# Kernel tuning notes

Measured on AMD Instinct MI355X. Metric: run time of the kernel, lower is better.

## Reference

```python
import jax, jax.numpy as jnp
import numpy as np

N_HEAD, N_KV, HEAD_DIM, GATE_CH = 16, 4, 128, 32

def _rope(x, cos, sin):
    d = x.shape[3] // 2
    x1, x2 = x[..., :d], x[..., d:]
    return jnp.concatenate([x1 * cos + x2 * sin, x1 * (-sin) + x2 * cos], axis=3)

def _rmsnorm(x):
    xf = x.astype(jnp.float32)
    return (x * jax.lax.rsqrt(jnp.mean(xf * xf, axis=-1, keepdims=True) + 1e-6)).astype(x.dtype)

def setup_inputs() -> dict:
    key = jax.random.key(0)
    ks = jax.random.split(key, 9)
    B, T, C = 2, 2048, 2048
    return {
        "x":  jax.random.normal(ks[0], (B, T, C), jnp.float32),
        "ve": jax.random.normal(ks[1], (B, T, N_KV * HEAD_DIM), jnp.float32),
        "cos": jax.random.uniform(ks[2], (T, 1, HEAD_DIM // 2), jnp.float32),
        "sin": jax.random.uniform(ks[3], (T, 1, HEAD_DIM // 2), jnp.float32),
        "Wq": jax.random.normal(ks[4], (C, N_HEAD * HEAD_DIM), jnp.float32) * 0.02,
        "Wk": jax.random.normal(ks[5], (C, N_KV * HEAD_DIM), jnp.float32) * 0.02,
        "Wv": jax.random.normal(ks[6], (C, N_KV * HEAD_DIM), jnp.float32) * 0.02,
        "Wg": jax.random.normal(ks[7], (GATE_CH, N_KV), jnp.float32) * 0.02,
        "Wo": jax.random.normal(ks[8], (C, C), jnp.float32) * 0.02,
        "window": 1024,
    }

def reference(x, ve, cos, sin, Wq, Wk, Wv, Wg, Wo, window):
    B, T, C = x.shape
    q = (x @ Wq).reshape(B, T, N_HEAD, HEAD_DIM)
    k = (x @ Wk).reshape(B, T, N_KV, HEAD_DIM)
    v = (x @ Wv).reshape(B, T, N_KV, HEAD_DIM)
    # value-embedding gate (ve_gate active for this layer)
    gate = 2.0 * jax.nn.sigmoid(x[..., :GATE_CH] @ Wg)  # (B,T,N_KV)
    v = v + gate[..., None] * ve.reshape(B, T, N_KV, HEAD_DIM)
    q, k = _rope(q, cos, sin), _rope(k, cos, sin)
    q, k = _rmsnorm(q), _rmsnorm(k)
    # GQA: repeat kv heads (repeat_interleave over head dim)
    groups = N_HEAD // N_KV
    k = jnp.repeat(k, groups, axis=2)
    v = jnp.repeat(v, groups, axis=2)
    scale = 1.0 / np.sqrt(HEAD_DIM)
    scores = jnp.einsum("bthd,bshd->bhts", q, k) * scale  # (B,H,T,T)
    idx = jnp.arange(T)
    diff = idx[None, :] - idx[:, None]  # diff[i,j] = j - i, as in torch code
    mask = (diff >= 0) & (diff < window)
    scores = jnp.where(mask[None, None], scores, -jnp.inf)
    p = jax.nn.softmax(scores, axis=-1)
    y = jnp.einsum("bhts,bshd->bthd", p, v).reshape(B, T, C)
    return y @ Wo
```

## Files before the change

kernel.cpp:

```cpp
#include <hip/hip_runtime.h>
#include <hip/hip_bf16.h>
#include <cstdint>

typedef __hip_bfloat16 bf16;
typedef __attribute__((ext_vector_type(8))) short short8;
typedef __attribute__((ext_vector_type(4))) float f32x4;

#define T_   2048
#define CDIM 2048
#define NH   16
#define NKV  4
#define HD   128
#define QSCALE (0.08838834764831845f * 1.44269504088896340f)

__device__ __forceinline__ void gload_lds16(const void* g, void* l) {
  __builtin_amdgcn_global_load_lds(
      (const __attribute__((address_space(1))) void*)g,
      (__attribute__((address_space(3))) void*)l, 16, 0, 0);
}

__global__ __launch_bounds__(256) void cast_x_kernel(const float4* __restrict__ in,
                                                     ushort4* __restrict__ out, int n4) {
  int i = blockIdx.x * 256 + threadIdx.x;
  if (i >= n4) return;
  float4 v = in[i];
  union { bf16 h[4]; ushort4 u; } cv;
  cv.h[0] = __float2bfloat16(v.x);
  cv.h[1] = __float2bfloat16(v.y);
  cv.h[2] = __float2bfloat16(v.z);
  cv.h[3] = __float2bfloat16(v.w);
  out[i] = cv.u;
}

__global__ __launch_bounds__(256) void cast_transpose(const float* __restrict__ W,
                                                      bf16* __restrict__ WT,
                                                      int K, int N) {
  __shared__ float tile[32][33];
  int k0 = blockIdx.y * 32, n0 = blockIdx.x * 32;
  int r = threadIdx.x >> 5, c = threadIdx.x & 31;
  for (int i = 0; i < 4; ++i)
    tile[r + i * 8][c] = W[(size_t)(k0 + r + i * 8) * N + n0 + c];
  __syncthreads();
  for (int i = 0; i < 4; ++i)
    WT[(size_t)(n0 + r + i * 8) * K + k0 + c] = __float2bfloat16(tile[c][r + i * 8]);
}

template <int MREP, typename CT>
__global__ __launch_bounds__(512, 2) void gemm_8p(const bf16* __restrict__ A,
                                                  const bf16* __restrict__ BT,
                                                  CT* __restrict__ C,
                                                  int N, int K, int RY, int RX) {
  constexpr int BM = MREP * 32;
  constexpr int ALOADS = BM / 64;
  __shared__ __align__(16) bf16 sA[2][BM * 64];
  __shared__ __align__(16) bf16 sB[2][256 * 64];

  int tid = threadIdx.x;
  int lane = tid & 63, w = tid >> 6;
  int wm = w >> 2, wn = w & 3;
  int lr = lane & 15, lk = lane >> 4;

  int xcd = blockIdx.x & 7, t = blockIdx.x >> 3;
  int by = (xcd >> 1) * RY + t / RX;
  int bx = (xcd & 1) * RX + t % RX;
  int m0 = by * BM, n0 = bx * 256;

  f32x4 acc[MREP][4];
#pragma unroll
  for (int m = 0; m < MREP; ++m)
#pragma unroll
    for (int n = 0; n < 4; ++n) acc[m][n] = (f32x4){0.f, 0.f, 0.f, 0.f};

  const bf16* Abase = A + (size_t)m0 * K;
  const bf16* Bbase = BT + (size_t)n0 * K;

  auto stage = [&](int b, int kt) {
    int kb = kt << 6;
#pragma unroll
    for (int i = 0; i < ALOADS; ++i) {
      int c = i * 512 + tid;
      int r = c >> 3, sl = c & 7;
      gload_lds16(Abase + (size_t)r * K + kb + ((sl ^ (r & 7)) << 3),
                  (char*)(&sA[b][0]) + c * 16);
    }
#pragma unroll
    for (int i = 0; i < 4; ++i) {
      int c = i * 512 + tid;
      int r = c >> 3, sl = c & 7;
      gload_lds16(Bbase + (size_t)r * K + kb + ((sl ^ (r & 7)) << 3),
                  (char*)(&sB[b][0]) + c * 16);
    }
  };

  int nk = K >> 6;
  stage(0, 0);
  stage(1, 1);
  if constexpr (MREP == 8)
    asm volatile("s_waitcnt vmcnt(8)\n\ts_barrier" ::: "memory");
  else
    asm volatile("s_waitcnt vmcnt(6)\n\ts_barrier" ::: "memory");

  for (int kt = 0; kt < nk; ++kt) {
    int d = kt & 1;
    const char* sAb = (const char*)(&sA[d][0]);
    const char* sBb = (const char*)(&sB[d][0]);

    short8 bfr[4][2];
#pragma unroll
    for (int n = 0; n < 4; ++n) {
      int row = wn * 64 + n * 16 + lr;
      const char* rb = sBb + row * 128;
      int rx = (row & 7) << 4;
      bfr[n][0] = *(const short8*)(rb + ((lk * 16) ^ rx));
      bfr[n][1] = *(const short8*)(rb + ((64 + lk * 16) ^ rx));
    }

#pragma unroll
    for (int p = 0; p < MREP / 2; ++p) {
      short8 af[2][2];
#pragma unroll
      for (int mi = 0; mi < 2; ++mi) {
        int row = wm * (MREP * 16) + (p * 2 + mi) * 16 + lr;
        const char* rb = sAb + row * 128;
        int rx = (row & 7) << 4;
        af[mi][0] = *(const short8*)(rb + ((lk * 16) ^ rx));
        af[mi][1] = *(const short8*)(rb + ((64 + lk * 16) ^ rx));
      }
      __builtin_amdgcn_s_setprio(1);
#pragma unroll
      for (int kk = 0; kk < 2; ++kk)
#pragma unroll
        for (int mi = 0; mi < 2; ++mi)
#pragma unroll
          for (int n = 0; n < 4; ++n)
            acc[p * 2 + mi][n] = __builtin_amdgcn_mfma_f32_16x16x32_bf16(
                af[mi][kk], bfr[n][kk], acc[p * 2 + mi][n], 0, 0, 0);
      __builtin_amdgcn_s_setprio(0);
    }

    asm volatile("s_waitcnt lgkmcnt(0)\n\ts_barrier" ::: "memory");
    if (kt + 2 < nk) {
      stage(d, kt + 2);
      if constexpr (MREP == 8)
        asm volatile("s_waitcnt vmcnt(8)\n\ts_barrier" ::: "memory");
      else
        asm volatile("s_waitcnt vmcnt(6)\n\ts_barrier" ::: "memory");
    } else {
      asm volatile("s_waitcnt vmcnt(0)\n\ts_barrier" ::: "memory");
    }
  }

#pragma unroll
  for (int m = 0; m < MREP; ++m)
#pragma unroll
    for (int n = 0; n < 4; ++n)
#pragma unroll
      for (int jj = 0; jj < 4; ++jj) {
        size_t idx = (size_t)(m0 + wm * (MREP * 16) + m * 16 + lk * 4 + jj) * N +
                     n0 + wn * 64 + n * 16 + lr;
        if constexpr (__is_same(CT, float))
          C[idx] = acc[m][n][jj];
        else
          C[idx] = __float2bfloat16(acc[m][n][jj]);
      }
}

__global__ __launch_bounds__(256) void epilogue_kernel(
    const bf16* __restrict__ qkv, const float* __restrict__ x,
    const float* __restrict__ ve, const float* __restrict__ cosT,
    const float* __restrict__ sinT, const float* __restrict__ Wg,
    bf16* __restrict__ qn, bf16* __restrict__ kn, bf16* __restrict__ vT) {
  int row = blockIdx.x;
  int bi = row >> 11, t = row & 2047;
  int tid = threadIdx.x, lane = tid & 63, w = tid >> 6;
  __shared__ float gate[NKV];
  size_t rb = (size_t)row * 3072;

  if (tid < 128) {
    int g = tid >> 5, i = tid & 31;
    float p = x[(size_t)row * CDIM + i] * Wg[i * 4 + g];
    p += __shfl_xor(p, 1);  p += __shfl_xor(p, 2);
    p += __shfl_xor(p, 4);  p += __shfl_xor(p, 8);
    p += __shfl_xor(p, 16);
    if (i == 0) gate[g] = 2.f / (1.f + __expf(-p));
  }
  __syncthreads();

  float cv = cosT[t * 64 + lane];
  float sv = sinT[t * 64 + lane];

  for (int it = 0; it < 4; ++it) {
    int h = it * 4 + w;
    float x1 = __bfloat162float(qkv[rb + h * 128 + lane]);
    float x2 = __bfloat162float(qkv[rb + h * 128 + 64 + lane]);
    float y1 = x1 * cv + x2 * sv;
    float y2 = x2 * cv - x1 * sv;
    float ss = y1 * y1 + y2 * y2;
    ss += __shfl_xor(ss, 1);  ss += __shfl_xor(ss, 2);  ss += __shfl_xor(ss, 4);
    ss += __shfl_xor(ss, 8);  ss += __shfl_xor(ss, 16); ss += __shfl_xor(ss, 32);
    float r = rsqrtf(ss * (1.f / 128.f) + 1e-6f) * QSCALE;
    size_t ob = (size_t)row * (NH * HD) + h * 128;
    qn[ob + lane] = __float2bfloat16(y1 * r);
    qn[ob + 64 + lane] = __float2bfloat16(y2 * r);
  }
  {
    int h = w;
    float x1 = __bfloat162float(qkv[rb + 2048 + h * 128 + lane]);
    float x2 = __bfloat162float(qkv[rb + 2048 + h * 128 + 64 + lane]);
    float y1 = x1 * cv + x2 * sv;
    float y2 = x2 * cv - x1 * sv;
    float ss = y1 * y1 + y2 * y2;
    ss += __shfl_xor(ss, 1);  ss += __shfl_xor(ss, 2);  ss += __shfl_xor(ss, 4);
    ss += __shfl_xor(ss, 8);  ss += __shfl_xor(ss, 16); ss += __shfl_xor(ss, 32);
    float r = rsqrtf(ss * (1.f / 128.f) + 1e-6f);
    size_t ob = (size_t)row * (NKV * HD) + h * 128;
    kn[ob + lane] = __float2bfloat16(y1 * r);
    kn[ob + 64 + lane] = __float2bfloat16(y2 * r);
  }
  for (int e = tid; e < 512; e += 256) {
    int kv = e >> 7, d = e & 127;
    float val = __bfloat162float(qkv[rb + 2560 + e]) + gate[kv] * ve[(size_t)row * 512 + e];
    vT[((size_t)(bi * NKV + kv) * HD + d) * T_ + t] = __float2bfloat16(val);
  }
}

__global__ __launch_bounds__(256) void attn_kernel(
    const bf16* __restrict__ qn, const bf16* __restrict__ kn,
    const bf16* __restrict__ vT, bf16* __restrict__ y,
    const int* __restrict__ winp) {
  __shared__ __align__(16) bf16 sK[2][64 * 128];
  __shared__ __align__(16) bf16 sV[2][128 * 64];
  __shared__ __align__(16) bf16 sP[4][16 * 64];

  int win = *winp;
  int id = blockIdx.x;
  int g  = id & 7;
  int bi = g >> 2;
  int kvh = g & 3;
  int rem = id >> 3;
  int h  = kvh * 4 + (rem & 3);
  int jslot = (rem >> 2) & 7;
  int s5 = rem >> 5;
  int q0i = (s5 == 0) ? (2 * jslot) : (s5 == 1) ? (2 * jslot + 1)
          : (s5 == 2) ? (16 + jslot) : (31 - jslot);
  int q0 = q0i << 6;
  int tid = threadIdx.x;
  int lane = tid & 63, w = tid >> 6;
  int lr = lane & 15, lk = lane >> 4;

  short8 qf[4];
  {
    const bf16* qrow = qn + (size_t)(bi * T_ + q0 + w * 16 + lr) * (NH * HD) + h * HD;
    for (int c = 0; c < 4; ++c) qf[c] = *(const short8*)(qrow + c * 32 + lk * 8);
  }

  f32x4 o[8];
  for (int i = 0; i < 8; ++i) o[i] = (f32x4){0.f, 0.f, 0.f, 0.f};
  float lpart[4] = {0.f, 0.f, 0.f, 0.f};

  int jt0 = q0 >> 6;
  int hi = q0 + 62 + win; if (hi > T_ - 1) hi = T_ - 1;
  int jt1 = hi >> 6;
  const float NEGINF = -__builtin_inff();

  char* sPb = (char*)(&sP[w][0]);
  int prx = (lr & 7) << 4;

  auto stageKV = [&](int b, int jtx) {
    int j0x = jtx << 6;
    for (int i = 0; i < 4; ++i) {
      int c = i * 256 + tid;
      int r = c >> 4, sl = c & 15;
      gload_lds16(kn + (size_t)(bi * T_ + j0x + r) * (NKV * HD) + kvh * HD + ((sl ^ (r & 7)) * 8),
                  (char*)(&sK[b][0]) + c * 16);
    }
    for (int i = 0; i < 4; ++i) {
      int c = i * 256 + tid;
      int r = c >> 3, sl = c & 7;
      gload_lds16(vT + ((size_t)(bi * NKV + kvh) * HD + r) * T_ + j0x + ((sl ^ (r & 7)) * 8),
                  (char*)(&sV[b][0]) + c * 16);
    }
  };

  stageKV(0, jt0);
  __syncthreads();

  int buf = 0;
  for (int jt = jt0; jt <= jt1; ++jt) {
    int j0 = jt << 6;
    if (jt < jt1) stageKV(buf ^ 1, jt + 1);

    const char* sKb = (const char*)(&sK[buf][0]);
    const char* sVb = (const char*)(&sV[buf][0]);

    f32x4 s[4];
    for (int sub = 0; sub < 4; ++sub) s[sub] = (f32x4){0.f, 0.f, 0.f, 0.f};
    for (int sub = 0; sub < 4; ++sub) {
      int kr = sub * 16 + lr;
      int rx = (kr & 7) << 4;
      const char* rowb = sKb + kr * 256;
      for (int c = 0; c < 4; ++c) {
        short8 kf = *(const short8*)(rowb + ((c * 64 + lk * 16) ^ rx));
        s[sub] = __builtin_amdgcn_mfma_f32_16x16x32_bf16(qf[c], kf, s[sub], 0, 0, 0);
      }
    }

    bool full = (j0 >= q0 + 64) && (j0 + 64 <= q0 + win);
    int ibase = q0 + w * 16 + lk * 4;

    for (int jj = 0; jj < 4; ++jj) {
      int irow = ibase + jj;
      int pr = lk * 4 + jj;
      int pwx = (pr & 7) << 4;
      char* pb = sPb + pr * 128;
      float v0, v1, v2, v3;
      if (full) {
        v0 = s[0][jj]; v1 = s[1][jj]; v2 = s[2][jj]; v3 = s[3][jj];
      } else {
        int j = j0 + lr;
        v0 = (j >= irow && j - irow < win)           ? s[0][jj] : NEGINF;
        v1 = (j + 16 >= irow && j + 16 - irow < win) ? s[1][jj] : NEGINF;
        v2 = (j + 32 >= irow && j + 32 - irow < win) ? s[2][jj] : NEGINF;
        v3 = (j + 48 >= irow && j + 48 - irow < win) ? s[3][jj] : NEGINF;
      }
      float p0 = exp2f(v0), p1 = exp2f(v1);
      float p2 = exp2f(v2), p3 = exp2f(v3);
      lpart[jj] += (p0 + p1) + (p2 + p3);
      *(bf16*)(pb + ((lr * 2)      ^ pwx)) = __float2bfloat16(p0);
      *(bf16*)(pb + ((32 + lr * 2) ^ pwx)) = __float2bfloat16(p1);
      *(bf16*)(pb + ((64 + lr * 2) ^ pwx)) = __float2bfloat16(p2);
      *(bf16*)(pb + ((96 + lr * 2) ^ pwx)) = __float2bfloat16(p3);
    }

    short8 pf0 = *(const short8*)(sPb + lr * 128 + ((lk * 16)      ^ prx));
    short8 pf1 = *(const short8*)(sPb + lr * 128 + ((64 + lk * 16) ^ prx));
    for (int nb = 0; nb < 8; ++nb) {
      int vr = nb * 16 + lr;
      int vrx = (vr & 7) << 4;
      const char* vb = sVb + vr * 128;
      short8 vf0 = *(const short8*)(vb + ((lk * 16)      ^ vrx));
      short8 vf1 = *(const short8*)(vb + ((64 + lk * 16) ^ vrx));
      o[nb] = __builtin_amdgcn_mfma_f32_16x16x32_bf16(pf0, vf0, o[nb], 0, 0, 0);
      o[nb] = __builtin_amdgcn_mfma_f32_16x16x32_bf16(pf1, vf1, o[nb], 0, 0, 0);
    }
    __syncthreads();
    buf ^= 1;
  }

  for (int jj = 0; jj < 4; ++jj) {
    float l = lpart[jj];
    l += __shfl_xor(l, 1); l += __shfl_xor(l, 2);
    l += __shfl_xor(l, 4); l += __shfl_xor(l, 8);
    float inv = 1.f / l;
    size_t ob = (size_t)(bi * T_ + q0 + w * 16 + lk * 4 + jj) * (NH * HD) + h * HD;
    for (int nb = 0; nb < 8; ++nb)
      y[ob + nb * 16 + lr] = __float2bfloat16(o[nb][jj] * inv);
  }
}

extern "C" void kernel_launch(void* const* d_in, const int* in_sizes, int n_in,
                              void* d_out, int out_size, void* d_ws, size_t ws_size,
                              hipStream_t stream) {
  const float* x    = (const float*)d_in[0];
  const float* ve   = (const float*)d_in[1];
  const float* cosT = (const float*)d_in[2];
  const float* sinT = (const float*)d_in[3];
  const float* Wq   = (const float*)d_in[4];
  const float* Wk   = (const float*)d_in[5];
  const float* Wv   = (const float*)d_in[6];
  const float* Wg   = (const float*)d_in[7];
  const float* Wo   = (const float*)d_in[8];
  const int*   win  = (const int*)d_in[9];
  float* out = (float*)d_out;

  char* ws = (char*)d_ws;
  bf16*  xb   = (bf16*)(ws);
  bf16*  wT   = (bf16*)(ws + 16777216);
  bf16*  woT  = (bf16*)(ws + 29360128);
  bf16*  qkvb = (bf16*)(ws + 37748736);
  bf16*  qn   = (bf16*)(ws + 62914560);
  bf16*  kn   = (bf16*)(ws + 79691776);
  bf16*  vTb  = (bf16*)(ws + 83886080);
  bf16*  y    = qkvb;

  cast_x_kernel<<<8192, 256, 0, stream>>>((const float4*)x, (ushort4*)xb, 2097152);
  cast_transpose<<<dim3(64, 64), 256, 0, stream>>>(Wq, wT, 2048, 2048);
  cast_transpose<<<dim3(16, 64), 256, 0, stream>>>(Wk, wT + (size_t)2048 * 2048, 2048, 512);
  cast_transpose<<<dim3(16, 64), 256, 0, stream>>>(Wv, wT + (size_t)2560 * 2048, 2048, 512);
  cast_transpose<<<dim3(64, 64), 256, 0, stream>>>(Wo, woT, 2048, 2048);

  gemm_8p<8, bf16><<<192, 512, 0, stream>>>(xb, wT, qkvb, 3072, 2048, 4, 6);
  epilogue_kernel<<<4096, 256, 0, stream>>>(qkvb, x, ve, cosT, sinT, Wg, qn, kn, vTb);
  attn_kernel<<<1024, 256, 0, stream>>>(qn, kn, vTb, y, win);
  gemm_8p<4, float><<<256, 512, 0, stream>>>(y, woT, out, 2048, 2048, 8, 4);
}
```

Before: 217.7 us.

## Add QKV GEMM kernel with per-quarter interleaved A-tile prefetch

Result: faster. 212.3 us (-2.5%).

```diff
diff --git a/kernel.cpp b/kernel.cpp
--- a/kernel.cpp
+++ b/kernel.cpp
@@ -45,6 +45,140 @@
     WT[(size_t)(n0 + r + i * 8) * K + k0 + c] = __float2bfloat16(tile[c][r + i * 8]);
 }
 
+__global__ __launch_bounds__(512, 2) void gemm_qkv8(const bf16* __restrict__ A,
+                                                    const bf16* __restrict__ BT,
+                                                    bf16* __restrict__ C,
+                                                    int N, int K, int RY, int RX) {
+  __shared__ __align__(16) bf16 sA[2][256 * 64];
+  __shared__ __align__(16) bf16 sB[2][256 * 64];
+
+  int tid = threadIdx.x;
+  int lane = tid & 63, w = tid >> 6;
+  int wm = w >> 2, wn = w & 3;
+  int lr = lane & 15, lk = lane >> 4;
+
+  int xcd = blockIdx.x & 7, t = blockIdx.x >> 3;
+  int by = (xcd >> 1) * RY + t / RX;
+  int bx = (xcd & 1) * RX + t % RX;
+  int m0 = by * 256, n0 = bx * 256;
+
+  f32x4 acc[8][4];
+#pragma unroll
+  for (int m = 0; m < 8; ++m)
+#pragma unroll
+    for (int n = 0; n < 4; ++n) acc[m][n] = (f32x4){0.f, 0.f, 0.f, 0.f};
+
+  const bf16* Abase = A + (size_t)m0 * K;
+  const bf16* Bbase = BT + (size_t)n0 * K;
+
+  auto stageB = [&](int p, int kt) {
+    int kb = kt << 6;
+#pragma unroll
+    for (int i = 0; i < 4; ++i) {
+      int c = i * 512 + tid;
+      int r = c >> 3, sl = c & 7;
+      gload_lds16(Bbase + (size_t)r * K + kb + ((sl ^ (r & 7)) << 3),
+                  (char*)(&sB[p][0]) + c * 16);
+    }
+  };
+  auto stageAq = [&](int p, int kt, int q) {
+    int kb = kt << 6;
+    int rbase = 32 * q + ((w & 3) << 3) + ((w >> 2) << 7);
+    int r = rbase + (lane >> 3), sl = lane & 7;
+    gload_lds16(Abase + (size_t)r * K + kb + ((sl ^ (r & 7)) << 3),
+                (char*)(&sA[p][0]) + rbase * 128 + lane * 16);
+  };
+
+  int nk = K >> 6;
+  stageB(0, 0);
+  stageAq(0, 0, 0); stageAq(0, 0, 1); stageAq(0, 0, 2); stageAq(0, 0, 3);
+  stageB(1, 1);
+  stageAq(1, 1, 0); stageAq(1, 1, 1); stageAq(1, 1, 2);
+  asm volatile("s_waitcnt vmcnt(7)" ::: "memory");
+  __builtin_amdgcn_s_barrier();
+
+#define READ_A(Q)                                                          \
+  {                                                                        \
+    _Pragma("unroll")                                                      \
+    for (int mi = 0; mi < 2; ++mi) {                                       \
+      int row = wm * 128 + (2 * (Q) + mi) * 16 + lr;                       \
+      const char* rb = sAb + row * 128;                                    \
+      int rx = (row & 7) << 4;                                             \
+      af[mi][0] = *(const short8*)(rb + ((lk * 16) ^ rx));                 \
+      af[mi][1] = *(const short8*)(rb + ((64 + lk * 16) ^ rx));            \
+    }                                                                      \
+  }
+#define MFMA_Q(Q)                                                          \
+  __builtin_amdgcn_s_setprio(1);                                          \
+  _Pragma("unroll")                                                        \
+  for (int kk = 0; kk < 2; ++kk)                                           \
+    _Pragma("unroll")                                                      \
+    for (int mi = 0; mi < 2; ++mi)                                         \
+      _Pragma("unroll")                                                    \
+      for (int n = 0; n < 4; ++n)                                          \
+        acc[2 * (Q) + mi][n] = __builtin_amdgcn_mfma_f32_16x16x32_bf16(    \
+            af[mi][kk], bfr[n][kk], acc[2 * (Q) + mi][n], 0, 0, 0);        \
+  __builtin_amdgcn_s_setprio(0);
+#define LGKM_FENCE                                                         \
+  asm volatile("s_waitcnt lgkmcnt(0)" ::: "memory");                       \
+  __builtin_amdgcn_sched_barrier(0);
+
+  for (int kt = 0; kt < nk; ++kt) {
+    int p = kt & 1;
+    const char* sAb = (const char*)(&sA[p][0]);
+    const char* sBb = (const char*)(&sB[p][0]);
+    short8 bfr[4][2], af[2][2];
+
+#pragma unroll
+    for (int n = 0; n < 4; ++n) {
+      int row = wn * 64 + n * 16 + lr;
+      const char* rb = sBb + row * 128;
+      int rx = (row & 7) << 4;
+      bfr[n][0] = *(const short8*)(rb + ((lk * 16) ^ rx));
+      bfr[n][1] = *(const short8*)(rb + ((64 + lk * 16) ^ rx));
+    }
+    READ_A(0);
+    if (kt + 1 < nk) stageAq(p ^ 1, kt + 1, 3);
+    LGKM_FENCE;
+    MFMA_Q(0);
+    __builtin_amdgcn_s_barrier();
+
+    READ_A(1);
+    if (kt + 2 < nk) { stageB(p, kt + 2); stageAq(p, kt + 2, 0); }
+    LGKM_FENCE;
+    MFMA_Q(1);
+    __builtin_amdgcn_s_barrier();
+
+    READ_A(2);
+    if (kt + 2 < nk) stageAq(p, kt + 2, 1);
+    LGKM_FENCE;
+    MFMA_Q(2);
+    __builtin_amdgcn_s_barrier();
+
+    READ_A(3);
+    if (kt + 2 < nk) stageAq(p, kt + 2, 2);
+    LGKM_FENCE;
+    MFMA_Q(3);
+    if (kt + 2 < nk)
+      asm volatile("s_waitcnt vmcnt(7)" ::: "memory");
+    else
+      asm volatile("s_waitcnt vmcnt(0)" ::: "memory");
+    __builtin_amdgcn_s_barrier();
+  }
+#undef READ_A
+#undef MFMA_Q
+#undef LGKM_FENCE
+
+#pragma unroll
+  for (int m = 0; m < 8; ++m)
+#pragma unroll
+    for (int n = 0; n < 4; ++n)
+#pragma unroll
+      for (int jj = 0; jj < 4; ++jj)
+        C[(size_t)(m0 + wm * 128 + m * 16 + lk * 4 + jj) * N +
+          n0 + wn * 64 + n * 16 + lr] = __float2bfloat16(acc[m][n][jj]);
+}
+
 template <int MREP, typename CT>
 __global__ __launch_bounds__(512, 2) void gemm_8p(const bf16* __restrict__ A,
                                                   const bf16* __restrict__ BT,
@@ -95,10 +229,8 @@
   int nk = K >> 6;
   stage(0, 0);
   stage(1, 1);
-  if constexpr (MREP == 8)
-    asm volatile("s_waitcnt vmcnt(8)\n\ts_barrier" ::: "memory");
-  else
-    asm volatile("s_waitcnt vmcnt(6)\n\ts_barrier" ::: "memory");
+  asm volatile("s_waitcnt vmcnt(6)" ::: "memory");
+  __builtin_amdgcn_s_barrier();
 
   for (int kt = 0; kt < nk; ++kt) {
     int d = kt & 1;
@@ -141,10 +273,7 @@
     asm volatile("s_waitcnt lgkmcnt(0)\n\ts_barrier" ::: "memory");
     if (kt + 2 < nk) {
       stage(d, kt + 2);
-      if constexpr (MREP == 8)
-        asm volatile("s_waitcnt vmcnt(8)\n\ts_barrier" ::: "memory");
-      else
-        asm volatile("s_waitcnt vmcnt(6)\n\ts_barrier" ::: "memory");
+      asm volatile("s_waitcnt vmcnt(6)\n\ts_barrier" ::: "memory");
     } else {
       asm volatile("s_waitcnt vmcnt(0)\n\ts_barrier" ::: "memory");
     }
@@ -389,7 +518,7 @@
   cast_transpose<<<dim3(16, 64), 256, 0, stream>>>(Wv, wT + (size_t)2560 * 2048, 2048, 512);
   cast_transpose<<<dim3(64, 64), 256, 0, stream>>>(Wo, woT, 2048, 2048);
 
-  gemm_8p<8, bf16><<<192, 512, 0, stream>>>(xb, wT, qkvb, 3072, 2048, 4, 6);
+  gemm_qkv8<<<192, 512, 0, stream>>>(xb, wT, qkvb, 3072, 2048, 4, 6);
   epilogue_kernel<<<4096, 256, 0, stream>>>(qkvb, x, ve, cosT, sinT, Wg, qn, kn, vTb);
   attn_kernel<<<1024, 256, 0, stream>>>(qn, kn, vTb, y, win);
   gemm_8p<4, float><<<256, 512, 0, stream>>>(y, woT, out, 2048, 2048, 8, 4);
```
